# Kernel tuning notes

Hardware: AMD Instinct MI355X
Metric: run time of the kernel (lower is better)

Reference implementation:

```python
import jax, jax.numpy as jnp
import numpy as np

LEVEL_SHAPES = ((128, 128), (64, 64), (32, 32), (16, 16))  # (H_l, W_l) per level
B, LQ, C, H, L, P, DFF = 4, 1024, 256, 8, 4, 4, 1024
DH = C // H
LSRC = sum(h * w for h, w in LEVEL_SHAPES)
NORMALIZER = np.array([[w, h] for h, w in LEVEL_SHAPES], dtype=np.float32)  # (L,2) as (W,H)


def layer_norm(x, g, b, eps=1e-5):
    m = jnp.mean(x, -1, keepdims=True)
    v = jnp.var(x, -1, keepdims=True)
    return (x - m) * jax.lax.rsqrt(v + eps) * g + b


def mha(tgt, query_pos, w_in, b_in, w_out, b_out):
    # nn.MultiheadAttention with q=k=tgt+pos, v=tgt (eval mode, no dropout)
    qk = tgt + query_pos
    q = (qk @ w_in[:C].T + b_in[:C]).reshape(B, LQ, H, DH)
    k = (qk @ w_in[C:2 * C].T + b_in[C:2 * C]).reshape(B, LQ, H, DH)
    v = (tgt @ w_in[2 * C:].T + b_in[2 * C:]).reshape(B, LQ, H, DH)
    att = jax.nn.softmax(jnp.einsum('bqhd,bkhd->bhqk', q, k) / np.float32(np.sqrt(DH)), axis=-1)
    o = jnp.einsum('bhqk,bkhd->bqhd', att, v).reshape(B, LQ, C)
    return o @ w_out.T + b_out


def ms_deform_attn(query, ref, src, off_w, off_b, aw_w, aw_b, val_w, val_b, out_w, out_b):
    value = (src @ val_w.T + val_b).reshape(B, LSRC, H, DH)
    offsets = (query @ off_w.T + off_b).reshape(B, LQ, H, L, P, 2)
    aw = jax.nn.softmax((query @ aw_w.T + aw_b).reshape(B, LQ, H, L * P), axis=-1)
    aw = aw.reshape(B, LQ, H, L, P)
    # sampling locations in [0,1], offsets normalized per level by (W_l, H_l)
    loc = ref[:, :, None, :, None, :] + offsets / NORMALIZER[None, None, None, :, None, :]
    out = jnp.zeros((B, LQ, H, DH), query.dtype)
    start = 0
    for l, (h, w) in enumerate(LEVEL_SHAPES):
        v = value[:, start:start + h * w].reshape(B, h, w, H, DH)
        v = v.transpose(0, 3, 1, 2, 4).reshape(B, H, h * w, DH)  # [B,H,hw,DH]
        start += h * w
        # grid_sample semantics: align_corners=False, zero padding
        x = loc[:, :, :, l, :, 0] * w - 0.5  # [B,LQ,H,P]
        y = loc[:, :, :, l, :, 1] * h - 0.5
        x0 = jnp.floor(x); y0 = jnp.floor(y)
        x0i = x0.astype(jnp.int32); y0i = y0.astype(jnp.int32)
        wx1 = x - x0; wx0 = 1.0 - wx1
        wy1 = y - y0; wy0 = 1.0 - wy1

        def gather(ix, iy):
            valid = ((ix >= 0) & (ix < w) & (iy >= 0) & (iy < h)).astype(v.dtype)
            idx = jnp.clip(iy, 0, h - 1) * w + jnp.clip(ix, 0, w - 1)
            idx = idx.transpose(0, 2, 1, 3).reshape(B, H, LQ * P)
            g = jnp.take_along_axis(v, idx[..., None], axis=2).reshape(B, H, LQ, P, DH)
            return g * valid.transpose(0, 2, 1, 3)[..., None]

        def wmul(ww):
            return ww.transpose(0, 2, 1, 3)[..., None]  # [B,H,LQ,P,1]

        s = (gather(x0i, y0i) * wmul(wx0 * wy0)
             + gather(x0i + 1, y0i) * wmul(wx1 * wy0)
             + gather(x0i, y0i + 1) * wmul(wx0 * wy1)
             + gather(x0i + 1, y0i + 1) * wmul(wx1 * wy1))
        out = out + jnp.einsum('bhqpd,bqhp->bqhd', s, aw[:, :, :, l])
    return out.reshape(B, LQ, C) @ out_w.T + out_b


def setup_inputs():
    key = jax.random.key(0)
    ks = jax.random.split(key, 16)

    def n(i, shape, s=0.02):
        return jax.random.normal(ks[i], shape, jnp.float32) * s

    z = lambda *s: jnp.zeros(s, jnp.float32)
    o = lambda *s: jnp.ones(s, jnp.float32)
    return {
        'tgt': n(0, (B, LQ, C), 1.0),
        'query_pos': n(1, (B, LQ, C), 1.0),
        'reference_points': jax.random.uniform(ks[2], (B, LQ, L, 2), jnp.float32),
        'src': n(3, (B, LSRC, C), 1.0),
        'in_w': n(4, (3 * C, C)), 'in_b': z(3 * C),
        'sa_w': n(5, (C, C)), 'sa_b': z(C),
        'off_w': n(6, (H * L * P * 2, C)), 'off_b': n(7, (H * L * P * 2,), 2.0),
        'aw_w': n(8, (H * L * P, C)), 'aw_b': z(H * L * P),
        'val_w': n(9, (C, C)), 'val_b': z(C),
        'co_w': n(10, (C, C)), 'co_b': z(C),
        'ln1_g': o(C), 'ln1_b': z(C),
        'ln2_g': o(C), 'ln2_b': z(C),
        'ln3_g': o(C), 'ln3_b': z(C),
        'f1_w': n(11, (DFF, C)), 'f1_b': z(DFF),
        'f2_w': n(12, (C, DFF)), 'f2_b': z(C),
    }


def reference(tgt, query_pos, reference_points, src, in_w, in_b, sa_w, sa_b,
              off_w, off_b, aw_w, aw_b, val_w, val_b, co_w, co_b,
              ln1_g, ln1_b, ln2_g, ln2_b, ln3_g, ln3_b,
              f1_w, f1_b, f2_w, f2_b):
    # self-attention + residual + norm2
    tgt2 = mha(tgt, query_pos, in_w, in_b, sa_w, sa_b)
    tgt = layer_norm(tgt + tgt2, ln2_g, ln2_b)
    # multi-scale deformable cross-attention + residual + norm1 (DETR path)
    tgt2 = ms_deform_attn(tgt + query_pos, reference_points, src,
                          off_w, off_b, aw_w, aw_b, val_w, val_b, co_w, co_b)
    tgt = layer_norm(tgt + tgt2, ln1_g, ln1_b)
    # FFN + residual + norm3
    tgt2 = jax.nn.relu(tgt @ f1_w.T + f1_b) @ f2_w.T + f2_b
    tgt = layer_norm(tgt + tgt2, ln3_g, ln3_b)
    return tgt
```

## Files before the change

### kernel.cpp

```cpp
#include <hip/hip_runtime.h>
#include <hip/hip_bf16.h>
#include <math.h>

#define Bv   4
#define LQv  1024
#define Cv   256
#define Hv   8
#define Lv   4
#define Pv   4
#define DFFv 1024
#define DHv  32
#define LSRCv 21760

typedef __attribute__((ext_vector_type(8))) short bhalf8;
typedef __attribute__((ext_vector_type(4))) float floatx4;

__device__ inline unsigned pk_bf16x2(float x, float y) {
    unsigned xb = __float_as_uint(x), yb = __float_as_uint(y);
    unsigned xr = (xb + 0x7FFFu + ((xb >> 16) & 1u)) >> 16;
    unsigned yr = (yb + 0x7FFFu + ((yb >> 16) & 1u)) >> 16;
    return xr | (yr << 16);
}
__device__ inline unsigned short bf16_1(float x) {
    unsigned xb = __float_as_uint(x);
    return (unsigned short)((xb + 0x7FFFu + ((xb >> 16) & 1u)) >> 16);
}
__device__ inline float ubf2f(unsigned short u) {
    return __uint_as_float(((unsigned)u) << 16);
}

__global__ __launch_bounds__(256) void cvt_weights(const float* __restrict__ in_w,
                                                   const float* __restrict__ sa_w,
                                                   const float* __restrict__ val_w,
                                                   const float* __restrict__ off_w,
                                                   const float* __restrict__ aw_w,
                                                   const float* __restrict__ co_w,
                                                   const float* __restrict__ f1_w,
                                                   const float* __restrict__ f2_w,
                                                   const float* __restrict__ off_b,
                                                   const float* __restrict__ aw_b,
                                                   unsigned short* __restrict__ wp,
                                                   float* __restrict__ cbias) {
    const size_t idx4 = (size_t)blockIdx.x * 256 + threadIdx.x;
    if (idx4 >= 253952) {
        const int t = (int)(idx4 - 253952);
        if (t < 256) cbias[t] = off_b[t];
        else if (t < 384) cbias[t] = aw_b[t - 256];
        return;
    }
    const size_t f = idx4 * 4;
    const float* src; size_t off; int K; size_t obase; int nadd = 0;
    if (f < 196608)      { src = in_w;  off = f;          K = 256;  obase = 0; }
    else if (f < 262144) { src = sa_w;  off = f - 196608; K = 256;  obase = 196608; }
    else if (f < 327680) { src = val_w; off = f - 262144; K = 256;  obase = 262144; }
    else if (f < 393216) { src = off_w; off = f - 327680; K = 256;  obase = 327680; }
    else if (f < 425984) { src = aw_w;  off = f - 393216; K = 256;  obase = 327680; nadd = 256; }
    else if (f < 491520) { src = co_w;  off = f - 425984; K = 256;  obase = 425984; }
    else if (f < 753664) { src = f1_w;  off = f - 491520; K = 256;  obase = 491520; }
    else                 { src = f2_w;  off = f - 753664; K = 1024; obase = 753664; }
    float4 v = *(const float4*)(src + off);
    const int n = (int)(off / (size_t)K) + nadd, k = (int)(off % (size_t)K);
    const size_t di = obase + ((size_t)((n >> 4) * (K >> 5) + (k >> 5))) * 512
                    + (size_t)(((k >> 3) & 3) * 128 + (n & 15) * 8 + (k & 7));
    *(uint2*)(wp + di) = (uint2){pk_bf16x2(v.x, v.y), pk_bf16x2(v.z, v.w)};
}

struct GJob {
    const float* A; const float* A2;
    const unsigned short* Wp; const float* bias;
    float* Cf; unsigned short* Ch;
    int M, N, K, relu;
};

__device__ __forceinline__ void gemm_body(unsigned short* AsBase,
                                          const float* __restrict__ A,
                                          const float* __restrict__ A2,
                                          const unsigned short* __restrict__ Wp,
                                          const float* __restrict__ bias,
                                          float* __restrict__ Cf,
                                          unsigned short* __restrict__ Ch,
                                          int N, int K, int relu, unsigned bid) {
    const unsigned nc = (unsigned)N >> 6;
    const unsigned xcd = bid & 7, j = bid >> 3;
    const unsigned cpan = j % nc, r8 = j / nc;
    const int bm = (int)((xcd + (r8 << 3)) << 6);
    const int bn = (int)(cpan << 6);
    const int tid = threadIdx.x;
    const int wid = tid >> 6, lane = tid & 63;
    const int wr = wid >> 1, wc = wid & 1;
    const int col16 = lane & 15;
    const int quad = lane >> 4;

    const int srow0 = tid >> 4;
    const int scol = (tid & 15) * 4;
    const float* asrc = A + (size_t)(bm + srow0) * K + scol;
    const float* a2src = A2 ? A2 + (size_t)(bm + srow0) * K + scol : nullptr;

    const int K32 = K >> 5;
    const unsigned short* wbase = Wp + ((size_t)((bn >> 4) + wc * 2) * K32) * 512
                                + (size_t)lane * 8;

    floatx4 acc[2][2] = {};
    float4 rv[4][2];

    auto loadA = [&](int c) {
#pragma unroll
        for (int j2 = 0; j2 < 4; ++j2)
#pragma unroll
            for (int i = 0; i < 2; ++i)
                rv[j2][i] = *(const float4*)(asrc + (size_t)(16 * j2) * K + c * 128 + 64 * i);
        if (a2src) {
#pragma unroll
            for (int j2 = 0; j2 < 4; ++j2)
#pragma unroll
                for (int i = 0; i < 2; ++i) {
                    float4 t = *(const float4*)(a2src + (size_t)(16 * j2) * K + c * 128 + 64 * i);
                    rv[j2][i].x += t.x; rv[j2][i].y += t.y;
                    rv[j2][i].z += t.z; rv[j2][i].w += t.w;
                }
        }
    };
    auto writeA = [&](int buf) {
        unsigned short* dst = AsBase + buf * (64 * 136);
#pragma unroll
        for (int j2 = 0; j2 < 4; ++j2)
#pragma unroll
            for (int i = 0; i < 2; ++i) {
                uint2 p = {pk_bf16x2(rv[j2][i].x, rv[j2][i].y),
                           pk_bf16x2(rv[j2][i].z, rv[j2][i].w)};
                *(uint2*)&dst[(srow0 + 16 * j2) * 136 + scol + 64 * i] = p;
            }
    };

    const int NC = K >> 7;
    loadA(0);
    writeA(0);

    for (int c = 0; c < NC; ++c) {
        __syncthreads();
        if (c + 1 < NC) loadA(c + 1);

        const unsigned short* ab = AsBase + (c & 1) * (64 * 136);
#pragma unroll
        for (int s = 0; s < 4; ++s) {
            bhalf8 bfr[2];
#pragma unroll
            for (int nt = 0; nt < 2; ++nt)
                bfr[nt] = *(const bhalf8*)(wbase + ((size_t)(nt * K32 + c * 4 + s)) * 512);
            bhalf8 af[2];
#pragma unroll
            for (int mt = 0; mt < 2; ++mt)
                af[mt] = *(const bhalf8*)&ab[(wr * 32 + mt * 16 + col16) * 136 + s * 32 + quad * 8];
#pragma unroll
            for (int mt = 0; mt < 2; ++mt)
#pragma unroll
                for (int nt = 0; nt < 2; ++nt)
                    acc[mt][nt] = __builtin_amdgcn_mfma_f32_16x16x32_bf16(
                        af[mt], bfr[nt], acc[mt][nt], 0, 0, 0);
        }

        if (c + 1 < NC) writeA((c + 1) & 1);
    }

#pragma unroll
    for (int mt = 0; mt < 2; ++mt) {
#pragma unroll
        for (int nt = 0; nt < 2; ++nt) {
            const int col = bn + wc * 32 + nt * 16 + col16;
            const float bv = bias[col];
#pragma unroll
            for (int i = 0; i < 4; ++i) {
                const int row = bm + wr * 32 + mt * 16 + quad * 4 + i;
                float v = acc[mt][nt][i] + bv;
                if (relu) v = fmaxf(v, 0.f);
                if (Ch) Ch[(size_t)row * N + col] = bf16_1(v);
                else    Cf[(size_t)row * N + col] = v;
            }
        }
    }
}

__global__ __launch_bounds__(256, 4) void gemm_single(const float* __restrict__ A,
                                                      const float* __restrict__ A2,
                                                      const unsigned short* __restrict__ Wp,
                                                      const float* __restrict__ bias,
                                                      float* __restrict__ Cf,
                                                      unsigned short* __restrict__ Ch,
                                                      int N, int K, int relu) {
    __shared__ __attribute__((aligned(16))) unsigned short As[2 * 64 * 136];
    gemm_body(As, A, A2, Wp, bias, Cf, Ch, N, K, relu, blockIdx.x);
}

__global__ __launch_bounds__(256, 4) void gemm_triple(GJob j0, GJob j1, GJob j2,
                                                      unsigned c0, unsigned c01) {
    __shared__ __attribute__((aligned(16))) unsigned short As[2 * 64 * 136];
    const unsigned b = blockIdx.x;
    if (b < c0) {
        gemm_body(As, j0.A, j0.A2, j0.Wp, j0.bias, j0.Cf, j0.Ch, j0.N, j0.K, j0.relu, b);
    } else if (b < c01) {
        gemm_body(As, j1.A, j1.A2, j1.Wp, j1.bias, j1.Cf, j1.Ch, j1.N, j1.K, j1.relu, b - c0);
    } else {
        gemm_body(As, j2.A, j2.A2, j2.Wp, j2.bias, j2.Cf, j2.Ch, j2.N, j2.K, j2.relu, b - c01);
    }
}

__global__ __launch_bounds__(256, 2) void gemm_ln(const float* __restrict__ A,
                                                  const unsigned short* __restrict__ Wp,
                                                  const float* __restrict__ bias,
                                                  const float* __restrict__ res,
                                                  const float* __restrict__ g,
                                                  const float* __restrict__ beta,
                                                  float* __restrict__ out,
                                                  int K) {
    __shared__ __attribute__((aligned(16))) unsigned short As[2][32 * 136];
    const int bm = blockIdx.x * 32;
    const int tid = threadIdx.x;
    const int wid = tid >> 6, lane = tid & 63;
    const int col16 = lane & 15, quad = lane >> 4;
    const int wc = wid;

    const int srow = tid >> 3;
    const int sc16 = (tid & 7) * 16;
    const float* asrc = A + (size_t)(bm + srow) * K + sc16;

    const int K32 = K >> 5;
    const unsigned short* wbase = Wp + (size_t)(wc * 4) * K32 * 512 + (size_t)lane * 8;

    floatx4 acc[2][4] = {};
    float4 rv[4];

    auto loadA = [&](int c) {
#pragma unroll
        for (int j = 0; j < 4; ++j)
            rv[j] = *(const float4*)(asrc + c * 128 + j * 4);
    };
    auto writeA = [&](int buf) {
#pragma unroll
        for (int j = 0; j < 4; ++j) {
            uint2 p = {pk_bf16x2(rv[j].x, rv[j].y), pk_bf16x2(rv[j].z, rv[j].w)};
            *(uint2*)&As[buf][srow * 136 + sc16 + j * 4] = p;
        }
    };

    const int NC = K >> 7;
    loadA(0);
    writeA(0);

    for (int c = 0; c < NC; ++c) {
        __syncthreads();
        if (c + 1 < NC) loadA(c + 1);

        const unsigned short* ab = As[c & 1];
#pragma unroll
        for (int s = 0; s < 4; ++s) {
            bhalf8 bfr[4];
#pragma unroll
            for (int nt = 0; nt < 4; ++nt)
                bfr[nt] = *(const bhalf8*)(wbase + ((size_t)(nt * K32 + c * 4 + s)) * 512);
            bhalf8 af[2];
#pragma unroll
            for (int mt = 0; mt < 2; ++mt)
                af[mt] = *(const bhalf8*)&ab[(mt * 16 + col16) * 136 + s * 32 + quad * 8];
#pragma unroll
            for (int mt = 0; mt < 2; ++mt)
#pragma unroll
                for (int nt = 0; nt < 4; ++nt)
                    acc[mt][nt] = __builtin_amdgcn_mfma_f32_16x16x32_bf16(
                        af[mt], bfr[nt], acc[mt][nt], 0, 0, 0);
        }

        if (c + 1 < NC) writeA((c + 1) & 1);
    }

    float bias_r[4];
#pragma unroll
    for (int nt = 0; nt < 4; ++nt) bias_r[nt] = bias[wc * 64 + nt * 16 + col16];

    float s_[2][4], q_[2][4];
#pragma unroll
    for (int mt = 0; mt < 2; ++mt)
#pragma unroll
        for (int i = 0; i < 4; ++i) { s_[mt][i] = 0.f; q_[mt][i] = 0.f; }

#pragma unroll
    for (int mt = 0; mt < 2; ++mt)
#pragma unroll
        for (int i = 0; i < 4; ++i) {
            const int row = bm + mt * 16 + quad * 4 + i;
#pragma unroll
            for (int nt = 0; nt < 4; ++nt) {
                float r = res[(size_t)row * 256 + wc * 64 + nt * 16 + col16];
                float v = acc[mt][nt][i] + bias_r[nt] + r;
                acc[mt][nt][i] = v;
                s_[mt][i] += v;
                q_[mt][i] = fmaf(v, v, q_[mt][i]);
            }
        }

#pragma unroll
    for (int mt = 0; mt < 2; ++mt)
#pragma unroll
        for (int i = 0; i < 4; ++i) {
#pragma unroll
            for (int off = 1; off < 16; off <<= 1) {
                s_[mt][i] += __shfl_xor(s_[mt][i], off, 64);
                q_[mt][i] += __shfl_xor(q_[mt][i], off, 64);
            }
        }

    __syncthreads();
    float* red = (float*)As;
    if (col16 == 0) {
#pragma unroll
        for (int mt = 0; mt < 2; ++mt)
#pragma unroll
            for (int i = 0; i < 4; ++i) {
                red[wid * 32 + mt * 16 + quad * 4 + i] = s_[mt][i];
                red[128 + wid * 32 + mt * 16 + quad * 4 + i] = q_[mt][i];
            }
    }
    __syncthreads();
    float* mean_s = red + 256;
    float* rstd_s = red + 288;
    if (tid < 32) {
        float S = red[tid] + red[32 + tid] + red[64 + tid] + red[96 + tid];
        float Q = red[128 + tid] + red[160 + tid] + red[192 + tid] + red[224 + tid];
        float mean = S * (1.f / 256.f);
        float var = Q * (1.f / 256.f) - mean * mean;
        mean_s[tid] = mean;
        rstd_s[tid] = rsqrtf(var + 1e-5f);
    }
    __syncthreads();

    float g_r[4], b_r[4];
#pragma unroll
    for (int nt = 0; nt < 4; ++nt) {
        g_r[nt] = g[wc * 64 + nt * 16 + col16];
        b_r[nt] = beta[wc * 64 + nt * 16 + col16];
    }
#pragma unroll
    for (int mt = 0; mt < 2; ++mt)
#pragma unroll
        for (int i = 0; i < 4; ++i) {
            const int rl = mt * 16 + quad * 4 + i;
            const float mn = mean_s[rl], rs = rstd_s[rl];
#pragma unroll
            for (int nt = 0; nt < 4; ++nt)
                out[(size_t)(bm + rl) * 256 + wc * 64 + nt * 16 + col16] =
                    (acc[mt][nt][i] - mn) * rs * g_r[nt] + b_r[nt];
        }
}

#define ATT_SCALE 0.17677669529663687f
__global__ __launch_bounds__(256, 2) void attn_mfma(const float* __restrict__ Q,
                                                    const float* __restrict__ Kb,
                                                    const float* __restrict__ Vb,
                                                    float* __restrict__ O,
                                                    int qk_stride) {
    const int b = blockIdx.z, h = blockIdx.y, qt = blockIdx.x;
    const int tid = threadIdx.x;
    const int wid = tid >> 6, lane = tid & 63;
    const int col16 = lane & 15, quad = lane >> 4;

    __shared__ unsigned short smem_us[40960];
    unsigned short* Ks = smem_us + wid * 9600;
    unsigned short* Vt = Ks + 2560;
    unsigned short* Ps = Ks + 4864;
    float* corr_s = (float*)(Ks + 9472);
    unsigned short* Qs = smem_us + 38400;

    {
        const int row = tid >> 2, part = tid & 3;
        const float* qsrc = Q + ((size_t)(b * LQv + qt * 64 + row)) * qk_stride + h * DHv + part * 8;
        float4 qa = *(const float4*)qsrc;
        float4 qb2 = *(const float4*)(qsrc + 4);
        uint4 qp = {pk_bf16x2(qa.x * ATT_SCALE, qa.y * ATT_SCALE),
                    pk_bf16x2(qa.z * ATT_SCALE, qa.w * ATT_SCALE),
                    pk_bf16x2(qb2.x * ATT_SCALE, qb2.y * ATT_SCALE),
                    pk_bf16x2(qb2.z * ATT_SCALE, qb2.w * ATT_SCALE)};
        *(uint4*)&Qs[row * 40 + part * 8] = qp;
    }
    __syncthreads();
    bhalf8 qfr[4];
#pragma unroll
    for (int j = 0; j < 4; ++j)
        qfr[j] = *(const bhalf8*)&Qs[(j * 16 + col16) * 40 + quad * 8];

    float m_state[4] = {-1e30f, -1e30f, -1e30f, -1e30f};
    float l_state[4] = {0.f, 0.f, 0.f, 0.f};
    floatx4 acc_o[4][2] = {};

    const float* kbase = Kb + ((size_t)(b * LQv + wid * 256)) * qk_stride + h * DHv;
    const float* vbase = Vb + ((size_t)(b * LQv + wid * 256)) * Cv + h * DHv;
    const int rsub = lane >> 3;
    const int c4 = (lane & 7) * 4;

#pragma unroll 1
    for (int t = 0; t < 4; ++t) {
        {
#pragma unroll
            for (int i = 0; i < 8; ++i) {
                const int row = i * 8 + rsub;
                const float4 f = *(const float4*)(kbase + (size_t)(t * 64 + row) * qk_stride + c4);
                *(uint2*)&Ks[row * 40 + c4] = (uint2){pk_bf16x2(f.x, f.y), pk_bf16x2(f.z, f.w)};
            }
        }
        {
#pragma unroll
            for (int i = 0; i < 8; ++i) {
                const int krow = i * 8 + rsub;
                const float4 f = *(const float4*)(vbase + (size_t)(t * 64 + krow) * Cv + c4);
                Vt[(c4 + 0) * 72 + krow] = bf16_1(f.x);
                Vt[(c4 + 1) * 72 + krow] = bf16_1(f.y);
                Vt[(c4 + 2) * 72 + krow] = bf16_1(f.z);
                Vt[(c4 + 3) * 72 + krow] = bf16_1(f.w);
            }
        }

        floatx4 accs[4][4] = {};
        bhalf8 af[4];
#pragma unroll
        for (int kf = 0; kf < 4; ++kf)
            af[kf] = *(const bhalf8*)&Ks[(kf * 16 + col16) * 40 + quad * 8];
#pragma unroll
        for (int kf = 0; kf < 4; ++kf)
#pragma unroll
            for (int qf = 0; qf < 4; ++qf)
                accs[kf][qf] = __builtin_amdgcn_mfma_f32_16x16x32_bf16(
                    af[kf], qfr[qf], accs[kf][qf], 0, 0, 0);

#pragma unroll
        for (int qf = 0; qf < 4; ++qf) {
            float tmax = -1e30f;
#pragma unroll
            for (int kf = 0; kf < 4; ++kf) {
                tmax = fmaxf(tmax, fmaxf(fmaxf(accs[kf][qf][0], accs[kf][qf][1]),
                                         fmaxf(accs[kf][qf][2], accs[kf][qf][3])));
            }
            tmax = fmaxf(tmax, __shfl_xor(tmax, 16));
            tmax = fmaxf(tmax, __shfl_xor(tmax, 32));
            float mnew = fmaxf(m_state[qf], tmax);
            float cr = __expf(m_state[qf] - mnew);
            m_state[qf] = mnew;
            float psum = 0.f;
#pragma unroll
            for (int kf = 0; kf < 4; ++kf) {
                float p0 = __expf(accs[kf][qf][0] - mnew);
                float p1 = __expf(accs[kf][qf][1] - mnew);
                float p2 = __expf(accs[kf][qf][2] - mnew);
                float p3 = __expf(accs[kf][qf][3] - mnew);
                psum += (p0 + p1) + (p2 + p3);
                uint2 pp = {pk_bf16x2(p0, p1), pk_bf16x2(p2, p3)};
                *(uint2*)&Ps[(qf * 16 + col16) * 72 + kf * 16 + quad * 4] = pp;
            }
            psum += __shfl_xor(psum, 16);
            psum += __shfl_xor(psum, 32);
            l_state[qf] = l_state[qf] * cr + psum;
            if (quad == 0) corr_s[qf * 16 + col16] = cr;
        }

#pragma unroll
        for (int mf = 0; mf < 4; ++mf) {
            float4 cv = *(const float4*)&corr_s[mf * 16 + quad * 4];
#pragma unroll
            for (int nf = 0; nf < 2; ++nf) {
                acc_o[mf][nf][0] *= cv.x;
                acc_o[mf][nf][1] *= cv.y;
                acc_o[mf][nf][2] *= cv.z;
                acc_o[mf][nf][3] *= cv.w;
            }
        }
#pragma unroll
        for (int ks2 = 0; ks2 < 2; ++ks2) {
            bhalf8 pf[4], vf[2];
#pragma unroll
            for (int mf = 0; mf < 4; ++mf)
                pf[mf] = *(const bhalf8*)&Ps[(mf * 16 + col16) * 72 + ks2 * 32 + quad * 8];
#pragma unroll
            for (int nf = 0; nf < 2; ++nf)
                vf[nf] = *(const bhalf8*)&Vt[(nf * 16 + col16) * 72 + ks2 * 32 + quad * 8];
#pragma unroll
            for (int mf = 0; mf < 4; ++mf)
#pragma unroll
                for (int nf = 0; nf < 2; ++nf)
                    acc_o[mf][nf] = __builtin_amdgcn_mfma_f32_16x16x32_bf16(
                        pf[mf], vf[nf], acc_o[mf][nf], 0, 0, 0);
        }
    }

    __syncthreads();
    float* mbuf = (float*)smem_us;
    float* lbuf = mbuf + 256;
    float* obuf = lbuf + 256;
    if (quad == 0) {
#pragma unroll
        for (int qf = 0; qf < 4; ++qf) {
            mbuf[wid * 64 + qf * 16 + col16] = m_state[qf];
            lbuf[wid * 64 + qf * 16 + col16] = l_state[qf];
        }
    }
#pragma unroll
    for (int mf = 0; mf < 4; ++mf)
#pragma unroll
        for (int nf = 0; nf < 2; ++nf)
#pragma unroll
            for (int i = 0; i < 4; ++i)
                obuf[wid * 2048 + (mf * 16 + quad * 4 + i) * 32 + nf * 16 + col16] =
                    acc_o[mf][nf][i];
    __syncthreads();
    {
        const int q = tid >> 2, dg = (tid & 3) * 8;
        float m0 = mbuf[q], m1 = mbuf[64 + q], m2 = mbuf[128 + q], m3 = mbuf[192 + q];
        float gm = fmaxf(fmaxf(m0, m1), fmaxf(m2, m3));
        float e0 = __expf(m0 - gm), e1 = __expf(m1 - gm);
        float e2 = __expf(m2 - gm), e3 = __expf(m3 - gm);
        float lt = lbuf[q] * e0 + lbuf[64 + q] * e1 + lbuf[128 + q] * e2 + lbuf[192 + q] * e3;
        float inv = 1.f / lt;
        const float* o0 = obuf + q * 32 + dg;
        float* orow = O + ((size_t)(b * LQv + qt * 64 + q)) * Cv + h * DHv + dg;
        float ov[8];
#pragma unroll
        for (int d = 0; d < 8; ++d)
            ov[d] = (o0[d] * e0 + o0[2048 + d] * e1 + o0[4096 + d] * e2 + o0[6144 + d] * e3) * inv;
        *(float4*)(orow) = make_float4(ov[0], ov[1], ov[2], ov[3]);
        *(float4*)(orow + 4) = make_float4(ov[4], ov[5], ov[6], ov[7]);
    }
}

__global__ __launch_bounds__(256) void deform_sample(const unsigned short* __restrict__ value,
                                                     const float* __restrict__ oab,
                                                     const float* __restrict__ ref,
                                                     float* __restrict__ out) {
    const int bq = blockIdx.x;
    const int b = bq >> 10;
    const int tid = threadIdx.x;
    const int h = tid >> 5, d = tid & 31;

    const float* aw = oab + (size_t)bq * 384 + 256 + h * 16;
    float w[16];
    float mx = -1e30f;
#pragma unroll
    for (int j = 0; j < 16; ++j) { w[j] = aw[j]; mx = fmaxf(mx, w[j]); }
    float ssum = 0.f;
#pragma unroll
    for (int j = 0; j < 16; ++j) { w[j] = __expf(w[j] - mx); ssum += w[j]; }
    float invs = 1.f / ssum;

    const float* op = oab + (size_t)bq * 384 + h * 32;
    const float* rp = ref + (size_t)bq * (Lv * 2);

    const int starts[4] = {0, 16384, 20480, 21504};
    const int WHl[4] = {128, 64, 32, 16};

    float acc = 0.f;
#pragma unroll 1
    for (int l = 0; l < 4; ++l) {
        const int wl = WHl[l];
        const float rx = rp[l * 2 + 0], ry = rp[l * 2 + 1];
        const unsigned short* vb0 = value + ((size_t)b * LSRCv + starts[l]) * Cv + h * DHv + d;
#pragma unroll 1
        for (int p = 0; p < 4; ++p) {
            float ox = op[l * 8 + p * 2 + 0], oy = op[l * 8 + p * 2 + 1];
            float x = rx * (float)wl + ox - 0.5f;
            float y = ry * (float)wl + oy - 0.5f;
            float fx0 = floorf(x), fy0 = floorf(y);
            int x0 = (int)fx0, y0 = (int)fy0;
            float tx = x - fx0, ty = y - fy0;
            float w00 = (1.f - tx) * (1.f - ty);
            float w10 = tx * (1.f - ty);
            float w01 = (1.f - tx) * ty;
            float w11 = tx * ty;
            float s = 0.f;
            bool xin0 = (x0 >= 0) & (x0 < wl);
            bool xin1 = (x0 + 1 >= 0) & (x0 + 1 < wl);
            bool yin0 = (y0 >= 0) & (y0 < wl);
            bool yin1 = (y0 + 1 >= 0) & (y0 + 1 < wl);
            if (yin0) {
                if (xin0) s = fmaf(w00, ubf2f(vb0[(size_t)(y0 * wl + x0) * Cv]), s);
                if (xin1) s = fmaf(w10, ubf2f(vb0[(size_t)(y0 * wl + x0 + 1) * Cv]), s);
            }
            if (yin1) {
                if (xin0) s = fmaf(w01, ubf2f(vb0[(size_t)((y0 + 1) * wl + x0) * Cv]), s);
                if (xin1) s = fmaf(w11, ubf2f(vb0[(size_t)((y0 + 1) * wl + x0 + 1) * Cv]), s);
            }
            acc = fmaf(w[l * 4 + p] * invs, s, acc);
        }
    }
    out[(size_t)bq * Cv + h * DHv + d] = acc;
}

extern "C" void kernel_launch(void* const* d_in, const int* in_sizes, int n_in,
                              void* d_out, int out_size, void* d_ws, size_t ws_size,
                              hipStream_t stream) {
    const float* tgt       = (const float*)d_in[0];
    const float* query_pos = (const float*)d_in[1];
    const float* ref_pts   = (const float*)d_in[2];
    const float* src       = (const float*)d_in[3];
    const float* in_w      = (const float*)d_in[4];
    const float* in_b      = (const float*)d_in[5];
    const float* sa_w      = (const float*)d_in[6];
    const float* sa_b      = (const float*)d_in[7];
    const float* off_w     = (const float*)d_in[8];
    const float* off_b     = (const float*)d_in[9];
    const float* aw_w      = (const float*)d_in[10];
    const float* aw_b      = (const float*)d_in[11];
    const float* val_w     = (const float*)d_in[12];
    const float* val_b     = (const float*)d_in[13];
    const float* co_w      = (const float*)d_in[14];
    const float* co_b      = (const float*)d_in[15];
    const float* ln1_g     = (const float*)d_in[16];
    const float* ln1_b     = (const float*)d_in[17];
    const float* ln2_g     = (const float*)d_in[18];
    const float* ln2_b     = (const float*)d_in[19];
    const float* ln3_g     = (const float*)d_in[20];
    const float* ln3_b     = (const float*)d_in[21];
    const float* f1_w      = (const float*)d_in[22];
    const float* f1_b      = (const float*)d_in[23];
    const float* f2_w      = (const float*)d_in[24];
    const float* f2_b      = (const float*)d_in[25];

    const int M0  = Bv * LQv * Cv;
    const int VSZ = Bv * LSRCv * Cv;
    float* ws = (float*)d_ws;

    float* big    = ws;
    float* qkbuf  = big;
    float* vb     = big + (size_t)2 * M0;
    float* ob     = big + (size_t)3 * M0;
    unsigned short* value16 = (unsigned short*)(big + (size_t)4 * M0);
    unsigned short* wb = (unsigned short*)(big + (size_t)20000000);
    float* cbias  = big + (size_t)20510000;
    float* tgt_a  = ws + (size_t)VSZ;
    float* oabuf  = tgt_a + M0;
    float* sampled= oabuf + (size_t)Bv * LQv * 384;
    float* tgt_b  = sampled + M0;
    float* hidden = tgt_b + M0;

    const size_t WB_IN = 0, WB_SA = 196608, WB_VAL = 262144, WB_OA = 327680,
                 WB_CO = 425984, WB_F1 = 491520, WB_F2 = 753664;

    const int Mq = Bv * LQv;
    dim3 blk256(256);

    cvt_weights<<<dim3(993), blk256, 0, stream>>>(
        in_w, sa_w, val_w, off_w, aw_w, co_w, f1_w, f2_w, off_b, aw_b, wb, cbias);

    {
        GJob jqk = {tgt, query_pos, wb + WB_IN, in_b, qkbuf, nullptr,
                    Mq, 512, Cv, 0};
        GJob jv  = {tgt, nullptr, wb + WB_IN + 131072, in_b + 2 * Cv, vb, nullptr,
                    Mq, Cv, Cv, 0};
        GJob jval= {src, nullptr, wb + WB_VAL, val_b, nullptr, value16,
                    Bv * LSRCv, Cv, Cv, 0};
        const unsigned c0 = (Mq / 64) * (512 / 64);
        const unsigned c1 = (Mq / 64) * (Cv / 64);
        const unsigned c2 = ((Bv * LSRCv) / 64) * (Cv / 64);
        gemm_triple<<<dim3(c0 + c1 + c2), blk256, 0, stream>>>(
            jqk, jv, jval, c0, c0 + c1);
    }

    attn_mfma<<<dim3(LQv / 64, Hv, Bv), blk256, 0, stream>>>(qkbuf, qkbuf + 256, vb, ob, 512);

    gemm_ln<<<dim3(Mq / 32), blk256, 0, stream>>>(
        ob, wb + WB_SA, sa_b, tgt, ln2_g, ln2_b, tgt_a, Cv);

    gemm_single<<<dim3((Mq / 64) * (384 / 64)), blk256, 0, stream>>>(
        tgt_a, query_pos, wb + WB_OA, cbias, oabuf, nullptr, 384, Cv, 0);

    deform_sample<<<dim3(Bv * LQv), blk256, 0, stream>>>(value16, oabuf, ref_pts, sampled);

    gemm_ln<<<dim3(Mq / 32), blk256, 0, stream>>>(
        sampled, wb + WB_CO, co_b, tgt_a, ln1_g, ln1_b, tgt_b, Cv);

    gemm_single<<<dim3((Mq / 64) * (DFFv / 64)), blk256, 0, stream>>>(
        tgt_b, nullptr, wb + WB_F1, f1_b, hidden, nullptr, DFFv, Cv, 1);

    gemm_ln<<<dim3(Mq / 32), blk256, 0, stream>>>(
        hidden, wb + WB_F2, f2_b, tgt_b, ln3_g, ln3_b, (float*)d_out, DFFv);
}
```

Before: 347.8 us.

## Emit bf16 intermediates and shrink gemm_ln row tile to 16

```diff
diff --git a/kernel.cpp b/kernel.cpp
--- a/kernel.cpp
+++ b/kernel.cpp
@@ -204,7 +204,7 @@
     }
 }
 
-__global__ __launch_bounds__(256, 2) void gemm_ln(const float* __restrict__ A,
+__global__ __launch_bounds__(256, 4) void gemm_ln(const unsigned short* __restrict__ Ah,
                                                   const unsigned short* __restrict__ Wp,
                                                   const float* __restrict__ bias,
                                                   const float* __restrict__ res,
@@ -212,35 +212,25 @@
                                                   const float* __restrict__ beta,
                                                   float* __restrict__ out,
                                                   int K) {
-    __shared__ __attribute__((aligned(16))) unsigned short As[2][32 * 136];
-    const int bm = blockIdx.x * 32;
+    __shared__ __attribute__((aligned(16))) unsigned short As[2][16 * 136];
+    const int bm = blockIdx.x * 16;
     const int tid = threadIdx.x;
     const int wid = tid >> 6, lane = tid & 63;
     const int col16 = lane & 15, quad = lane >> 4;
     const int wc = wid;
 
-    const int srow = tid >> 3;
-    const int sc16 = (tid & 7) * 16;
-    const float* asrc = A + (size_t)(bm + srow) * K + sc16;
+    const int srow = tid >> 4;
+    const int sc8 = (tid & 15) * 8;
+    const unsigned short* asrc = Ah + (size_t)(bm + srow) * K + sc8;
 
     const int K32 = K >> 5;
     const unsigned short* wbase = Wp + (size_t)(wc * 4) * K32 * 512 + (size_t)lane * 8;
 
-    floatx4 acc[2][4] = {};
-    float4 rv[4];
-
-    auto loadA = [&](int c) {
-#pragma unroll
-        for (int j = 0; j < 4; ++j)
-            rv[j] = *(const float4*)(asrc + c * 128 + j * 4);
-    };
-    auto writeA = [&](int buf) {
-#pragma unroll
-        for (int j = 0; j < 4; ++j) {
-            uint2 p = {pk_bf16x2(rv[j].x, rv[j].y), pk_bf16x2(rv[j].z, rv[j].w)};
-            *(uint2*)&As[buf][srow * 136 + sc16 + j * 4] = p;
-        }
-    };
+    floatx4 acc[4] = {};
+    uint4 rvh;
+
+    auto loadA = [&](int c) { rvh = *(const uint4*)(asrc + c * 128); };
+    auto writeA = [&](int buf) { *(uint4*)&As[buf][srow * 136 + sc8] = rvh; };
 
     const int NC = K >> 7;
     loadA(0);
@@ -257,16 +247,11 @@
 #pragma unroll
             for (int nt = 0; nt < 4; ++nt)
                 bfr[nt] = *(const bhalf8*)(wbase + ((size_t)(nt * K32 + c * 4 + s)) * 512);
-            bhalf8 af[2];
-#pragma unroll
-            for (int mt = 0; mt < 2; ++mt)
-                af[mt] = *(const bhalf8*)&ab[(mt * 16 + col16) * 136 + s * 32 + quad * 8];
-#pragma unroll
-            for (int mt = 0; mt < 2; ++mt)
-#pragma unroll
-                for (int nt = 0; nt < 4; ++nt)
-                    acc[mt][nt] = __builtin_amdgcn_mfma_f32_16x16x32_bf16(
-                        af[mt], bfr[nt], acc[mt][nt], 0, 0, 0);
+            bhalf8 af = *(const bhalf8*)&ab[col16 * 136 + s * 32 + quad * 8];
+#pragma unroll
+            for (int nt = 0; nt < 4; ++nt)
+                acc[nt] = __builtin_amdgcn_mfma_f32_16x16x32_bf16(
+                    af, bfr[nt], acc[nt], 0, 0, 0);
         }
 
         if (c + 1 < NC) writeA((c + 1) & 1);
@@ -276,55 +261,44 @@
 #pragma unroll
     for (int nt = 0; nt < 4; ++nt) bias_r[nt] = bias[wc * 64 + nt * 16 + col16];
 
-    float s_[2][4], q_[2][4];
-#pragma unroll
-    for (int mt = 0; mt < 2; ++mt)
-#pragma unroll
-        for (int i = 0; i < 4; ++i) { s_[mt][i] = 0.f; q_[mt][i] = 0.f; }
-
-#pragma unroll
-    for (int mt = 0; mt < 2; ++mt)
-#pragma unroll
-        for (int i = 0; i < 4; ++i) {
-            const int row = bm + mt * 16 + quad * 4 + i;
-#pragma unroll
-            for (int nt = 0; nt < 4; ++nt) {
-                float r = res[(size_t)row * 256 + wc * 64 + nt * 16 + col16];
-                float v = acc[mt][nt][i] + bias_r[nt] + r;
-                acc[mt][nt][i] = v;
-                s_[mt][i] += v;
-                q_[mt][i] = fmaf(v, v, q_[mt][i]);
-            }
-        }
-
-#pragma unroll
-    for (int mt = 0; mt < 2; ++mt)
-#pragma unroll
-        for (int i = 0; i < 4; ++i) {
-#pragma unroll
-            for (int off = 1; off < 16; off <<= 1) {
-                s_[mt][i] += __shfl_xor(s_[mt][i], off, 64);
-                q_[mt][i] += __shfl_xor(q_[mt][i], off, 64);
-            }
-        }
+    float s_[4] = {}, q_[4] = {};
+#pragma unroll
+    for (int i = 0; i < 4; ++i) {
+        const int row = bm + quad * 4 + i;
+#pragma unroll
+        for (int nt = 0; nt < 4; ++nt) {
+            float r = res[(size_t)row * 256 + wc * 64 + nt * 16 + col16];
+            float v = acc[nt][i] + bias_r[nt] + r;
+            acc[nt][i] = v;
+            s_[i] += v;
+            q_[i] = fmaf(v, v, q_[i]);
+        }
+    }
+
+#pragma unroll
+    for (int i = 0; i < 4; ++i) {
+#pragma unroll
+        for (int off = 1; off < 16; off <<= 1) {
+            s_[i] += __shfl_xor(s_[i], off, 64);
+            q_[i] += __shfl_xor(q_[i], off, 64);
+        }
+    }
 
     __syncthreads();
     float* red = (float*)As;
     if (col16 == 0) {
 #pragma unroll
-        for (int mt = 0; mt < 2; ++mt)
-#pragma unroll
-            for (int i = 0; i < 4; ++i) {
-                red[wid * 32 + mt * 16 + quad * 4 + i] = s_[mt][i];
-                red[128 + wid * 32 + mt * 16 + quad * 4 + i] = q_[mt][i];
-            }
+        for (int i = 0; i < 4; ++i) {
+            red[wid * 16 + quad * 4 + i] = s_[i];
+            red[64 + wid * 16 + quad * 4 + i] = q_[i];
+        }
     }
     __syncthreads();
-    float* mean_s = red + 256;
-    float* rstd_s = red + 288;
-    if (tid < 32) {
-        float S = red[tid] + red[32 + tid] + red[64 + tid] + red[96 + tid];
-        float Q = red[128 + tid] + red[160 + tid] + red[192 + tid] + red[224 + tid];
+    float* mean_s = red + 128;
+    float* rstd_s = red + 144;
+    if (tid < 16) {
+        float S = red[tid] + red[16 + tid] + red[32 + tid] + red[48 + tid];
+        float Q = red[64 + tid] + red[80 + tid] + red[96 + tid] + red[112 + tid];
         float mean = S * (1.f / 256.f);
         float var = Q * (1.f / 256.f) - mean * mean;
         mean_s[tid] = mean;
@@ -339,23 +313,21 @@
         b_r[nt] = beta[wc * 64 + nt * 16 + col16];
     }
 #pragma unroll
-    for (int mt = 0; mt < 2; ++mt)
-#pragma unroll
-        for (int i = 0; i < 4; ++i) {
-            const int rl = mt * 16 + quad * 4 + i;
-            const float mn = mean_s[rl], rs = rstd_s[rl];
-#pragma unroll
-            for (int nt = 0; nt < 4; ++nt)
-                out[(size_t)(bm + rl) * 256 + wc * 64 + nt * 16 + col16] =
-                    (acc[mt][nt][i] - mn) * rs * g_r[nt] + b_r[nt];
-        }
+    for (int i = 0; i < 4; ++i) {
+        const int rl = quad * 4 + i;
+        const float mn = mean_s[rl], rs = rstd_s[rl];
+#pragma unroll
+        for (int nt = 0; nt < 4; ++nt)
+            out[(size_t)(bm + rl) * 256 + wc * 64 + nt * 16 + col16] =
+                (acc[nt][i] - mn) * rs * g_r[nt] + b_r[nt];
+    }
 }
 
 #define ATT_SCALE 0.17677669529663687f
 __global__ __launch_bounds__(256, 2) void attn_mfma(const float* __restrict__ Q,
                                                     const float* __restrict__ Kb,
                                                     const float* __restrict__ Vb,
-                                                    float* __restrict__ O,
+                                                    unsigned short* __restrict__ O,
                                                     int qk_stride) {
     const int b = blockIdx.z, h = blockIdx.y, qt = blockIdx.x;
     const int tid = threadIdx.x;
@@ -517,20 +489,21 @@
         float lt = lbuf[q] * e0 + lbuf[64 + q] * e1 + lbuf[128 + q] * e2 + lbuf[192 + q] * e3;
         float inv = 1.f / lt;
         const float* o0 = obuf + q * 32 + dg;
-        float* orow = O + ((size_t)(b * LQv + qt * 64 + q)) * Cv + h * DHv + dg;
+        unsigned short* orow = O + ((size_t)(b * LQv + qt * 64 + q)) * Cv + h * DHv + dg;
         float ov[8];
 #pragma unroll
         for (int d = 0; d < 8; ++d)
             ov[d] = (o0[d] * e0 + o0[2048 + d] * e1 + o0[4096 + d] * e2 + o0[6144 + d] * e3) * inv;
-        *(float4*)(orow) = make_float4(ov[0], ov[1], ov[2], ov[3]);
-        *(float4*)(orow + 4) = make_float4(ov[4], ov[5], ov[6], ov[7]);
+        uint4 op = {pk_bf16x2(ov[0], ov[1]), pk_bf16x2(ov[2], ov[3]),
+                    pk_bf16x2(ov[4], ov[5]), pk_bf16x2(ov[6], ov[7])};
+        *(uint4*)orow = op;
     }
 }
 
 __global__ __launch_bounds__(256) void deform_sample(const unsigned short* __restrict__ value,
                                                      const float* __restrict__ oab,
                                                      const float* __restrict__ ref,
-                                                     float* __restrict__ out) {
+                                                     unsigned short* __restrict__ out) {
     const int bq = blockIdx.x;
     const int b = bq >> 10;
     const int tid = threadIdx.x;
@@ -586,7 +559,7 @@
             acc = fmaf(w[l * 4 + p] * invs, s, acc);
         }
     }
-    out[(size_t)bq * Cv + h * DHv + d] = acc;
+    out[(size_t)bq * Cv + h * DHv + d] = bf16_1(acc);
 }
 
 extern "C" void kernel_launch(void* const* d_in, const int* in_sizes, int n_in,
@@ -626,15 +599,15 @@
     float* big    = ws;
     float* qkbuf  = big;
     float* vb     = big + (size_t)2 * M0;
-    float* ob     = big + (size_t)3 * M0;
+    unsigned short* ob16 = (unsigned short*)(big + (size_t)3 * M0);
     unsigned short* value16 = (unsigned short*)(big + (size_t)4 * M0);
     unsigned short* wb = (unsigned short*)(big + (size_t)20000000);
     float* cbias  = big + (size_t)20510000;
     float* tgt_a  = ws + (size_t)VSZ;
     float* oabuf  = tgt_a + M0;
-    float* sampled= oabuf + (size_t)Bv * LQv * 384;
-    float* tgt_b  = sampled + M0;
-    float* hidden = tgt_b + M0;
+    unsigned short* sampled16 = (unsigned short*)(oabuf + (size_t)Bv * LQv * 384);
+    float* tgt_b  = (float*)(sampled16 + M0);
+    unsigned short* hidden16 = (unsigned short*)(tgt_b + M0);
 
     const size_t WB_IN = 0, WB_SA = 196608, WB_VAL = 262144, WB_OA = 327680,
                  WB_CO = 425984, WB_F1 = 491520, WB_F2 = 753664;
@@ -659,22 +632,22 @@
             jqk, jv, jval, c0, c0 + c1);
     }
 
-    attn_mfma<<<dim3(LQv / 64, Hv, Bv), blk256, 0, stream>>>(qkbuf, qkbuf + 256, vb, ob, 512);
-
-    gemm_ln<<<dim3(Mq / 32), blk256, 0, stream>>>(
-        ob, wb + WB_SA, sa_b, tgt, ln2_g, ln2_b, tgt_a, Cv);
+    attn_mfma<<<dim3(LQv / 64, Hv, Bv), blk256, 0, stream>>>(qkbuf, qkbuf + 256, vb, ob16, 512);
+
+    gemm_ln<<<dim3(Mq / 16), blk256, 0, stream>>>(
+        ob16, wb + WB_SA, sa_b, tgt, ln2_g, ln2_b, tgt_a, Cv);
 
     gemm_single<<<dim3((Mq / 64) * (384 / 64)), blk256, 0, stream>>>(
         tgt_a, query_pos, wb + WB_OA, cbias, oabuf, nullptr, 384, Cv, 0);
 
-    deform_sample<<<dim3(Bv * LQv), blk256, 0, stream>>>(value16, oabuf, ref_pts, sampled);
-
-    gemm_ln<<<dim3(Mq / 32), blk256, 0, stream>>>(
-        sampled, wb + WB_CO, co_b, tgt_a, ln1_g, ln1_b, tgt_b, Cv);
+    deform_sample<<<dim3(Bv * LQv), blk256, 0, stream>>>(value16, oabuf, ref_pts, sampled16);
+
+    gemm_ln<<<dim3(Mq / 16), blk256, 0, stream>>>(
+        sampled16, wb + WB_CO, co_b, tgt_a, ln1_g, ln1_b, tgt_b, Cv);
 
     gemm_single<<<dim3((Mq / 64) * (DFFv / 64)), blk256, 0, stream>>>(
-        tgt_b, nullptr, wb + WB_F1, f1_b, hidden, nullptr, DFFv, Cv, 1);
-
-    gemm_ln<<<dim3(Mq / 32), blk256, 0, stream>>>(
-        hidden, wb + WB_F2, f2_b, tgt_b, ln3_g, ln3_b, (float*)d_out, DFFv);
-}
+        tgt_b, nullptr, wb + WB_F1, f1_b, nullptr, hidden16, DFFv, Cv, 1);
+
+    gemm_ln<<<dim3(Mq / 16), blk256, 0, stream>>>(
+        hidden16, wb + WB_F2, f2_b, tgt_b, ln3_g, ln3_b, (float*)d_out, DFFv);
+}
```

After: 341.2 us. No clear change (-1.9%).
